# Optimization experiments

Hardware: AMD Instinct MI355X
Metric: run time of the kernel (lower is better)

The kernel has to match this reference:

```python
import jax, jax.numpy as jnp
import numpy as np

H_STEPS = 30 * 24 * 12
HID = 128
BATCH = 16


def setup_inputs() -> dict:
    key = jax.random.key(0)
    ks = jax.random.split(key, 16)
    s = 1.0 / np.sqrt(HID)  # PyTorch LSTM/Linear init scale
    u = lambda k, shape: jax.random.uniform(k, shape, jnp.float32, -s, s)
    return {
        "y0": jax.random.normal(ks[0], (BATCH, 1, 1), jnp.float32),
        "h0": jax.random.normal(ks[1], (2, BATCH, HID), jnp.float32),
        "c0": jax.random.normal(ks[2], (2, BATCH, HID), jnp.float32),
        "W_ih0": u(ks[3], (4 * HID, 1)),
        "W_hh0": u(ks[4], (4 * HID, HID)),
        "b_ih0": u(ks[5], (4 * HID,)),
        "b_hh0": u(ks[6], (4 * HID,)),
        "W_ih1": u(ks[7], (4 * HID, HID)),
        "W_hh1": u(ks[8], (4 * HID, HID)),
        "b_ih1": u(ks[9], (4 * HID,)),
        "b_hh1": u(ks[10], (4 * HID,)),
        "fc_w": u(ks[11], (1, HID)),
        "fc_b": u(ks[12], (1,)),
    }


def _lstm_cell(x, h, c, Wi, Wh, bi, bh):
    # PyTorch gate order: i, f, g, o
    gates = x @ Wi.T + bi + h @ Wh.T + bh  # [B, 4H]
    i, f, g, o = jnp.split(gates, 4, axis=-1)
    c_new = jax.nn.sigmoid(f) * c + jax.nn.sigmoid(i) * jnp.tanh(g)
    h_new = jax.nn.sigmoid(o) * jnp.tanh(c_new)
    return h_new, c_new


def reference(y0, h0, c0, W_ih0, W_hh0, b_ih0, b_hh0,
              W_ih1, W_hh1, b_ih1, b_hh1, fc_w, fc_b):
    def step(carry, _):
        y, h0_, c0_, h1_, c1_ = carry  # y: [B,1]
        h0n, c0n = _lstm_cell(y, h0_, c0_, W_ih0, W_hh0, b_ih0, b_hh0)
        h1n, c1n = _lstm_cell(h0n, h1_, c1_, W_ih1, W_hh1, b_ih1, b_hh1)
        yn = h1n @ fc_w.T + fc_b  # [B,1]
        return (yn, h0n, c0n, h1n, c1n), yn

    carry0 = (y0[:, 0, :], h0[0], c0[0], h0[1], c0[1])
    _, ys = jax.lax.scan(step, carry0, None, length=H_STEPS)  # [H, B, 1]
    return jnp.transpose(ys, (1, 0, 2))  # [B, H, 1]
```

## Files before the change

### kernel.cpp

```cpp
#include <hip/hip_runtime.h>

#define HSTEPS 8640
#define HID 128
#define BATCH 16
#define NTHR 512
#define YRING 192
#define INV127 (1.0f / 127.0f)

typedef __attribute__((ext_vector_type(4))) int i32x4;

static __device__ __forceinline__ float sigm(float x) {
    return __builtin_amdgcn_rcpf(1.0f + __expf(-x));
}
template <int CTRL>
static __device__ __forceinline__ float dppmov(float x) {
    return __int_as_float(
        __builtin_amdgcn_mov_dpp(__float_as_int(x), CTRL, 0xF, 0xF, false));
}
static __device__ __forceinline__ float sum4(float x) {
    x += dppmov<0x121>(x);
    x += dppmov<0x122>(x);
    return x;
}
static __device__ __forceinline__ float red_wave(float x) {
    x += dppmov<0x121>(x);
    x += dppmov<0x122>(x);
    x += dppmov<0x124>(x);
    x += dppmov<0x128>(x);
    float t1 = __int_as_float(__builtin_amdgcn_update_dpp(
        0, __float_as_int(x), 0x142 , 0xA, 0xF, false));
    x += t1;
    float t2 = __int_as_float(__builtin_amdgcn_update_dpp(
        0, __float_as_int(x), 0x143 , 0xC, 0xF, false));
    x += t2;
    return x;
}
static __device__ __forceinline__ float maxwave(float x) {
    x = fmaxf(x, dppmov<0x121>(x));
    x = fmaxf(x, dppmov<0x122>(x));
    x = fmaxf(x, dppmov<0x124>(x));
    x = fmaxf(x, dppmov<0x128>(x));
    float t1 = __int_as_float(__builtin_amdgcn_update_dpp(
        0, __float_as_int(x), 0x142, 0xA, 0xF, false));
    x = fmaxf(x, t1);
    float t2 = __int_as_float(__builtin_amdgcn_update_dpp(
        0, __float_as_int(x), 0x143, 0xC, 0xF, false));
    x = fmaxf(x, t2);
    return x;
}
static __device__ __forceinline__ float swzx16(float x) {
    return __int_as_float(
        __builtin_amdgcn_ds_swizzle(__float_as_int(x), 0x401F));
}

static __device__ __forceinline__ int pack4(const float* v, float inv) {
    int a = (int)__builtin_rintf(v[0] * inv);
    int b = (int)__builtin_rintf(v[1] * inv);
    int c = (int)__builtin_rintf(v[2] * inv);
    int d = (int)__builtin_rintf(v[3] * inv);
    return (a & 0xff) | ((b & 0xff) << 8) | ((c & 0xff) << 16) |
           ((d & 0xff) << 24);
}

static __device__ __forceinline__ void quantrow(const float* rp, int grp,
                                                i32x4& f0, i32x4& f1,
                                                float& sw) {
    float v[32];
#pragma unroll
    for (int j = 0; j < 16; ++j) v[j] = rp[16 * grp + j];
#pragma unroll
    for (int j = 0; j < 16; ++j) v[16 + j] = rp[64 + 16 * grp + j];
    float mx = 1e-20f;
#pragma unroll
    for (int j = 0; j < 32; ++j) mx = fmaxf(mx, __builtin_fabsf(v[j]));
    mx = fmaxf(mx, swzx16(mx));
    mx = fmaxf(mx, __shfl_xor(mx, 32, 64));
    float inv = 127.0f / mx;
    sw = mx * INV127;
    f0 = i32x4{pack4(v, inv), pack4(v + 4, inv), pack4(v + 8, inv),
               pack4(v + 12, inv)};
    f1 = i32x4{pack4(v + 16, inv), pack4(v + 20, inv), pack4(v + 24, inv),
               pack4(v + 28, inv)};
}

#define LOADT(M, T, FA, FB, SS)                                               \
    quantrow((M) + (size_t)(128 * ((T) >> 1) + 16 * (2 * gw + ((T) & 1)) +    \
                            ln15) * HID,                                      \
             grp, FA, FB, SS);

#define CH2(Q, A0, A1, FA, FB)                                                \
    Q = __builtin_amdgcn_mfma_i32_16x16x64_i8((A0), FA, zqi, 0, 0, 0);        \
    Q = __builtin_amdgcn_mfma_i32_16x16x64_i8((A1), FB, (Q), 0, 0, 0);

__global__ __launch_bounds__(NTHR, 2) void lstm2_kernel(
    const float* __restrict__ y0, const float* __restrict__ h0in,
    const float* __restrict__ c0in, const float* __restrict__ Wih0,
    const float* __restrict__ Whh0, const float* __restrict__ bih0,
    const float* __restrict__ bhh0, const float* __restrict__ Wih1,
    const float* __restrict__ Whh1, const float* __restrict__ bih1,
    const float* __restrict__ bhh1, const float* __restrict__ fcw,
    const float* __restrict__ fcb, float* __restrict__ out) {
    const int b = blockIdx.x;
    const int t = threadIdx.x;
    const int wv = t >> 6;
    const int ln = t & 63;
    const int grp = ln >> 4;
    const int ln15 = ln & 15;
    const int gw = wv & 3;
    const bool isX = wv < 4;
    const int jj = ln >> 5;
    const bool isBt = (ln & 16) != 0;
    const int e = 32 * gw + 16 * jj + ln15;
    const float foldc = isBt ? 2.0f : 1.0f;
    const int g1 = isBt ? 2 : 0;

    __shared__ __align__(16) char hsm8[512];
    __shared__ float ypartbuf[4];
    __shared__ float maxb[8];
    __shared__ float ybuf[YRING];

    const i32x4 zqi = {0, 0, 0, 0};

    i32x4 Fq0 = zqi, Fq1 = zqi, Fq2 = zqi, Fq3 = zqi, Fq4 = zqi, Fq5 = zqi,
          Fq6 = zqi, Fq7 = zqi, Fq8 = zqi, Fq9 = zqi, Fq10 = zqi, Fq11 = zqi,
          Fq12 = zqi, Fq13 = zqi, Fq14 = zqi, Fq15 = zqi, Fq16 = zqi,
          Fq17 = zqi, Fq18 = zqi, Fq19 = zqi, Fq20 = zqi, Fq21 = zqi,
          Fq22 = zqi, Fq23 = zqi, Fq24 = zqi, Fq25 = zqi, Fq26 = zqi,
          Fq27 = zqi, Fq28 = zqi, Fq29 = zqi, Fq30 = zqi, Fq31 = zqi;
    i32x4 QA0 = zqi, QA1 = zqi, QA2 = zqi, QA3 = zqi, QA4 = zqi, QA5 = zqi,
          QA6 = zqi, QA7 = zqi;
    i32x4 QB0 = zqi, QB1 = zqi, QB2 = zqi, QB3 = zqi, QB4 = zqi, QB5 = zqi,
          QB6 = zqi, QB7 = zqi;
    float B1c = 0, B2c = 0;
    float E1c = 0, E2c = 0;
    float SAb1 = 0, SAb2 = 0;
    float SAq1 = 0, SAq2 = 0;
    float SBb1 = 0, SBb2 = 0;
    float SBq1 = 0, SBq2 = 0;
    float Cst = 0;

    if (isX) {
        float S0, S1, S2, S3, S4, S5, S6, S7;
        LOADT(Whh0, 0, Fq0, Fq1, S0) LOADT(Whh0, 1, Fq2, Fq3, S1)
        LOADT(Whh0, 2, Fq4, Fq5, S2) LOADT(Whh0, 3, Fq6, Fq7, S3)
        LOADT(Whh0, 4, Fq8, Fq9, S4) LOADT(Whh0, 5, Fq10, Fq11, S5)
        LOADT(Whh0, 6, Fq12, Fq13, S6) LOADT(Whh0, 7, Fq14, Fq15, S7)
        SAb1 = (isBt ? (jj ? S5 : S4) : (jj ? S1 : S0)) * foldc;
        SAb2 = isBt ? (jj ? S7 : S6) : (jj ? S3 : S2);
        B1c = (bih0[g1 * 128 + e] + bhh0[g1 * 128 + e]) * foldc;
        B2c = bih0[(g1 + 1) * 128 + e] + bhh0[(g1 + 1) * 128 + e];
        E1c = Wih0[g1 * 128 + e] * foldc;
        E2c = Wih0[(g1 + 1) * 128 + e];
        Cst = isBt ? 0.f : c0in[b * HID + e];
    } else {
        float S0, S1, S2, S3, S4, S5, S6, S7, S8, S9, S10, S11, S12, S13,
            S14, S15;
        LOADT(Wih1, 0, Fq0, Fq1, S0) LOADT(Wih1, 1, Fq2, Fq3, S1)
        LOADT(Wih1, 2, Fq4, Fq5, S2) LOADT(Wih1, 3, Fq6, Fq7, S3)
        LOADT(Wih1, 4, Fq8, Fq9, S4) LOADT(Wih1, 5, Fq10, Fq11, S5)
        LOADT(Wih1, 6, Fq12, Fq13, S6) LOADT(Wih1, 7, Fq14, Fq15, S7)
        LOADT(Whh1, 0, Fq16, Fq17, S8) LOADT(Whh1, 1, Fq18, Fq19, S9)
        LOADT(Whh1, 2, Fq20, Fq21, S10) LOADT(Whh1, 3, Fq22, Fq23, S11)
        LOADT(Whh1, 4, Fq24, Fq25, S12) LOADT(Whh1, 5, Fq26, Fq27, S13)
        LOADT(Whh1, 6, Fq28, Fq29, S14) LOADT(Whh1, 7, Fq30, Fq31, S15)
        SAq1 = (isBt ? (jj ? S5 : S4) : (jj ? S1 : S0)) * foldc * INV127;
        SAq2 = (isBt ? (jj ? S7 : S6) : (jj ? S3 : S2)) * INV127;
        SBb1 = (isBt ? (jj ? S13 : S12) : (jj ? S9 : S8)) * foldc;
        SBb2 = isBt ? (jj ? S15 : S14) : (jj ? S11 : S10);
        B1c = (bih1[g1 * 128 + e] + bhh1[g1 * 128 + e]) * foldc;
        B2c = bih1[(g1 + 1) * 128 + e] + bhh1[(g1 + 1) * 128 + e];
        E1c = isBt ? 0.f : fcw[e];
        Cst = isBt ? 0.f : c0in[(BATCH + b) * HID + e];
    }

    const float fcb_ = fcb[0];

    float hv_ = 0.f;
    if (t < 128) hv_ = h0in[b * HID + t];
    else if (t < 256) hv_ = h0in[(BATCH + b) * HID + (t - 128)];
    float am = maxwave(__builtin_fabsf(hv_));
    if (ln == 63) maxb[wv] = am;
    if (t < 4) ypartbuf[t] = (t == 0) ? (y0[b] - fcb_) : 0.0f;
    __syncthreads();
    const float bm0 = fmaxf(fmaxf(maxb[0], maxb[1]), 1e-20f);
    const float bm1 = fmaxf(fmaxf(maxb[2], maxb[3]), 1e-20f);
    if (t < 128)
        hsm8[t] = (char)(int)__builtin_rintf(hv_ * (127.0f / bm0));
    else if (t < 256)
        hsm8[256 + (t - 128)] = (char)(int)__builtin_rintf(hv_ * (127.0f / bm1));
    __syncthreads();

    if (isX) {
        SAq1 = SAb1 * (bm0 * INV127);
        SAq2 = SAb2 * (bm0 * INV127);
    } else {
        SBq1 = SBb1 * (bm1 * INV127);
        SBq2 = SBb2 * (bm1 * INV127);
    }

    float* outb = out + (size_t)b * HSTEPS;

    if (isX) {
        i32x4 a0 = *(const i32x4*)&hsm8[16 * grp];
        i32x4 a1 = *(const i32x4*)&hsm8[64 + 16 * grp];
        CH2(QA0, a0, a1, Fq0, Fq1) CH2(QA1, a0, a1, Fq2, Fq3)
        CH2(QA2, a0, a1, Fq4, Fq5) CH2(QA3, a0, a1, Fq6, Fq7)
        CH2(QA4, a0, a1, Fq8, Fq9) CH2(QA5, a0, a1, Fq10, Fq11)
        CH2(QA6, a0, a1, Fq12, Fq13) CH2(QA7, a0, a1, Fq14, Fq15)
    }

    int p = 0;
    int ys = 0;
    int flush_at = YRING;

#pragma unroll 1
    for (int s = 0; s < HSTEPS; ++s) {
        if (isX) {
            float yv = sum4(ypartbuf[ln & 3]) + fcb_;
            if (s > 0) {
                if (t == 0) ybuf[ys] = yv;
                ys = (ys == YRING - 1) ? 0 : ys + 1;
            }
            int a1 = isBt ? (jj ? QA5[0] : QA4[0]) : (jj ? QA1[0] : QA0[0]);
            int a2 = isBt ? (jj ? QA7[0] : QA6[0]) : (jj ? QA3[0] : QA2[0]);
            float G1 = __builtin_fmaf(SAq1, (float)a1,
                                      __builtin_fmaf(E1c, yv, B1c));
            float G2 = __builtin_fmaf(SAq2, (float)a2,
                                      __builtin_fmaf(E2c, yv, B2c));
            float v1 = sigm(G1);
            float v2 = sigm(G2);
            float tg = __builtin_fmaf(2.f, swzx16(v1), -1.f);
            Cst = __builtin_fmaf(v2, Cst, v1 * tg);
            float v3 = sigm(2.f * Cst);
            float th = __builtin_fmaf(2.f, v3, -1.f);
            float h0n = swzx16(v2) * th;
            if (!(ln & 16))
                hsm8[(p ^ 1) * 128 + e] =
                    (char)(int)__builtin_rintf(h0n * 127.0f);
            if (s == 0) {
                SAq1 = SAb1 * INV127;
                SAq2 = SAb2 * INV127;
            }
        } else {
            const char* h1p = hsm8 + 256 + 128 * p + 16 * grp;
            i32x4 b0_ = *(const i32x4*)(h1p);
            i32x4 b1_ = *(const i32x4*)(h1p + 64);
            CH2(QB0, b0_, b1_, Fq16, Fq17) CH2(QB1, b0_, b1_, Fq18, Fq19)
            CH2(QB2, b0_, b1_, Fq20, Fq21) CH2(QB3, b0_, b1_, Fq22, Fq23)
            CH2(QB4, b0_, b1_, Fq24, Fq25) CH2(QB5, b0_, b1_, Fq26, Fq27)
            CH2(QB6, b0_, b1_, Fq28, Fq29) CH2(QB7, b0_, b1_, Fq30, Fq31)
        }
        __syncthreads();

        if (isX) {
            if (s == flush_at) {
                if (t < YRING) outb[flush_at - YRING + t] = ybuf[t];
                flush_at += YRING;
            }
            const char* h0np = hsm8 + (p ^ 1) * 128 + 16 * grp;
            i32x4 d0 = *(const i32x4*)(h0np);
            i32x4 d1 = *(const i32x4*)(h0np + 64);
            CH2(QA0, d0, d1, Fq0, Fq1) CH2(QA1, d0, d1, Fq2, Fq3)
            CH2(QA2, d0, d1, Fq4, Fq5) CH2(QA3, d0, d1, Fq6, Fq7)
            CH2(QA4, d0, d1, Fq8, Fq9) CH2(QA5, d0, d1, Fq10, Fq11)
            CH2(QA6, d0, d1, Fq12, Fq13) CH2(QA7, d0, d1, Fq14, Fq15)
        } else {
            __builtin_amdgcn_s_setprio(1);
            const char* h0np = hsm8 + (p ^ 1) * 128 + 16 * grp;
            i32x4 d0 = *(const i32x4*)(h0np);
            i32x4 d1 = *(const i32x4*)(h0np + 64);
            CH2(QA0, d0, d1, Fq0, Fq1) CH2(QA1, d0, d1, Fq2, Fq3)
            CH2(QA2, d0, d1, Fq4, Fq5) CH2(QA3, d0, d1, Fq6, Fq7)
            CH2(QA4, d0, d1, Fq8, Fq9) CH2(QA5, d0, d1, Fq10, Fq11)
            CH2(QA6, d0, d1, Fq12, Fq13) CH2(QA7, d0, d1, Fq14, Fq15)
            int a1 = isBt ? (jj ? QA5[0] : QA4[0]) : (jj ? QA1[0] : QA0[0]);
            int a2 = isBt ? (jj ? QA7[0] : QA6[0]) : (jj ? QA3[0] : QA2[0]);
            int c1 = isBt ? (jj ? QB5[0] : QB4[0]) : (jj ? QB1[0] : QB0[0]);
            int c2 = isBt ? (jj ? QB7[0] : QB6[0]) : (jj ? QB3[0] : QB2[0]);
            float H1 = __builtin_fmaf(
                SAq1, (float)a1,
                __builtin_fmaf(SBq1, (float)c1, B1c));
            float H2 = __builtin_fmaf(
                SAq2, (float)a2,
                __builtin_fmaf(SBq2, (float)c2, B2c));
            float v1 = sigm(H1);
            float v2 = sigm(H2);
            float tg = __builtin_fmaf(2.f, swzx16(v1), -1.f);
            Cst = __builtin_fmaf(v2, Cst, v1 * tg);
            float v3 = sigm(2.f * Cst);
            float th = __builtin_fmaf(2.f, v3, -1.f);
            float h1n = swzx16(v2) * th;
            __builtin_amdgcn_s_setprio(0);
            if (!(ln & 16))
                hsm8[256 + (p ^ 1) * 128 + e] =
                    (char)(int)__builtin_rintf(h1n * 127.0f);
            float part = red_wave(E1c * h1n);
            if (ln == 63) ypartbuf[gw] = part;
            if (s == 0) {
                SBq1 = SBb1 * INV127;
                SBq2 = SBb2 * INV127;
            }
        }
        __syncthreads();
        p ^= 1;
    }

    if (isX) {
        float yv = sum4(ypartbuf[ln & 3]) + fcb_;
        if (t == 0) ybuf[YRING - 1] = yv;
    }
    __syncthreads();
    if (t < YRING) outb[HSTEPS - YRING + t] = ybuf[t];
}

extern "C" void kernel_launch(void* const* d_in, const int* in_sizes, int n_in,
                              void* d_out, int out_size, void* d_ws,
                              size_t ws_size, hipStream_t stream) {
    const float* y0 = (const float*)d_in[0];
    const float* h0 = (const float*)d_in[1];
    const float* c0 = (const float*)d_in[2];
    const float* Wih0 = (const float*)d_in[3];
    const float* Whh0 = (const float*)d_in[4];
    const float* bih0 = (const float*)d_in[5];
    const float* bhh0 = (const float*)d_in[6];
    const float* Wih1 = (const float*)d_in[7];
    const float* Whh1 = (const float*)d_in[8];
    const float* bih1 = (const float*)d_in[9];
    const float* bhh1 = (const float*)d_in[10];
    const float* fcw = (const float*)d_in[11];
    const float* fcb = (const float*)d_in[12];
    float* out = (float*)d_out;

    lstm2_kernel<<<dim3(BATCH), dim3(NTHR), 0, stream>>>(
        y0, h0, c0, Wih0, Whh0, bih0, bhh0, Wih1, Whh1, bih1, bhh1, fcw, fcb,
        out);
}
```

Baseline: 6.604 ms.

## Quantize layer-1 weights with a shared scale and accumulate both matmuls in MFMA

Layer-1 W_ih1 and W_hh1 rows now share a single int8 scale per row, so the recurrent h1 contribution and the h0 contribution can be summed inside the same int32 MFMA accumulator (the second chain continues from the first instead of being converted separately). This removes a second accumulator set, separate scale factors and extra int-to-float converts and FMAs on the critical layer-1 path. The step-0 term, which uses a different h1 scale, is precomputed before the loop and fed in as a bias. The cost is coarser quantization for whichever matrix has the smaller magnitudes, which may reduce accuracy.

```diff
diff --git a/kernel.cpp b/kernel.cpp
--- a/kernel.cpp
+++ b/kernel.cpp
@@ -83,13 +83,47 @@
                pack4(v + 28, inv)};
 }
 
-#define LOADT(M, T, FA, FB, SS)                                               \
-    quantrow((M) + (size_t)(128 * ((T) >> 1) + 16 * (2 * gw + ((T) & 1)) +    \
-                            ln15) * HID,                                      \
-             grp, FA, FB, SS);
+static __device__ __forceinline__ void quantrow2(const float* rpA,
+                                                 const float* rpB, int grp,
+                                                 i32x4& a0, i32x4& a1,
+                                                 i32x4& b0, i32x4& b1,
+                                                 float& sw) {
+    float vA[32], vB[32];
+#pragma unroll
+    for (int j = 0; j < 16; ++j) {
+        vA[j] = rpA[16 * grp + j];
+        vA[16 + j] = rpA[64 + 16 * grp + j];
+        vB[j] = rpB[16 * grp + j];
+        vB[16 + j] = rpB[64 + 16 * grp + j];
+    }
+    float mx = 1e-20f;
+#pragma unroll
+    for (int j = 0; j < 32; ++j) {
+        mx = fmaxf(mx, __builtin_fabsf(vA[j]));
+        mx = fmaxf(mx, __builtin_fabsf(vB[j]));
+    }
+    mx = fmaxf(mx, swzx16(mx));
+    mx = fmaxf(mx, __shfl_xor(mx, 32, 64));
+    float inv = 127.0f / mx;
+    sw = mx * INV127;
+    a0 = i32x4{pack4(vA, inv), pack4(vA + 4, inv), pack4(vA + 8, inv),
+               pack4(vA + 12, inv)};
+    a1 = i32x4{pack4(vA + 16, inv), pack4(vA + 20, inv), pack4(vA + 24, inv),
+               pack4(vA + 28, inv)};
+    b0 = i32x4{pack4(vB, inv), pack4(vB + 4, inv), pack4(vB + 8, inv),
+               pack4(vB + 12, inv)};
+    b1 = i32x4{pack4(vB + 16, inv), pack4(vB + 20, inv), pack4(vB + 24, inv),
+               pack4(vB + 28, inv)};
+}
+
+#define ROWOFF(T) \
+    ((size_t)(128 * ((T) >> 1) + 16 * (2 * gw + ((T) & 1)) + ln15) * HID)
 
 #define CH2(Q, A0, A1, FA, FB)                                                \
     Q = __builtin_amdgcn_mfma_i32_16x16x64_i8((A0), FA, zqi, 0, 0, 0);        \
+    Q = __builtin_amdgcn_mfma_i32_16x16x64_i8((A1), FB, (Q), 0, 0, 0);
+#define CH2C(Q, A0, A1, FA, FB)                                               \
+    Q = __builtin_amdgcn_mfma_i32_16x16x64_i8((A0), FA, (Q), 0, 0, 0);        \
     Q = __builtin_amdgcn_mfma_i32_16x16x64_i8((A1), FB, (Q), 0, 0, 0);
 
 __global__ __launch_bounds__(NTHR, 2) void lstm2_kernel(
@@ -127,24 +161,25 @@
           Fq17 = zqi, Fq18 = zqi, Fq19 = zqi, Fq20 = zqi, Fq21 = zqi,
           Fq22 = zqi, Fq23 = zqi, Fq24 = zqi, Fq25 = zqi, Fq26 = zqi,
           Fq27 = zqi, Fq28 = zqi, Fq29 = zqi, Fq30 = zqi, Fq31 = zqi;
-    i32x4 QA0 = zqi, QA1 = zqi, QA2 = zqi, QA3 = zqi, QA4 = zqi, QA5 = zqi,
-          QA6 = zqi, QA7 = zqi;
-    i32x4 QB0 = zqi, QB1 = zqi, QB2 = zqi, QB3 = zqi, QB4 = zqi, QB5 = zqi,
-          QB6 = zqi, QB7 = zqi;
+    i32x4 Q0 = zqi, Q1 = zqi, Q2 = zqi, Q3 = zqi, Q4 = zqi, Q5 = zqi,
+          Q6 = zqi, Q7 = zqi;
     float B1c = 0, B2c = 0;
     float E1c = 0, E2c = 0;
     float SAb1 = 0, SAb2 = 0;
     float SAq1 = 0, SAq2 = 0;
-    float SBb1 = 0, SBb2 = 0;
-    float SBq1 = 0, SBq2 = 0;
+    float HB1 = 0, HB2 = 0;
     float Cst = 0;
 
     if (isX) {
         float S0, S1, S2, S3, S4, S5, S6, S7;
-        LOADT(Whh0, 0, Fq0, Fq1, S0) LOADT(Whh0, 1, Fq2, Fq3, S1)
-        LOADT(Whh0, 2, Fq4, Fq5, S2) LOADT(Whh0, 3, Fq6, Fq7, S3)
-        LOADT(Whh0, 4, Fq8, Fq9, S4) LOADT(Whh0, 5, Fq10, Fq11, S5)
-        LOADT(Whh0, 6, Fq12, Fq13, S6) LOADT(Whh0, 7, Fq14, Fq15, S7)
+        quantrow(Whh0 + ROWOFF(0), grp, Fq0, Fq1, S0);
+        quantrow(Whh0 + ROWOFF(1), grp, Fq2, Fq3, S1);
+        quantrow(Whh0 + ROWOFF(2), grp, Fq4, Fq5, S2);
+        quantrow(Whh0 + ROWOFF(3), grp, Fq6, Fq7, S3);
+        quantrow(Whh0 + ROWOFF(4), grp, Fq8, Fq9, S4);
+        quantrow(Whh0 + ROWOFF(5), grp, Fq10, Fq11, S5);
+        quantrow(Whh0 + ROWOFF(6), grp, Fq12, Fq13, S6);
+        quantrow(Whh0 + ROWOFF(7), grp, Fq14, Fq15, S7);
         SAb1 = (isBt ? (jj ? S5 : S4) : (jj ? S1 : S0)) * foldc;
         SAb2 = isBt ? (jj ? S7 : S6) : (jj ? S3 : S2);
         B1c = (bih0[g1 * 128 + e] + bhh0[g1 * 128 + e]) * foldc;
@@ -153,20 +188,27 @@
         E2c = Wih0[(g1 + 1) * 128 + e];
         Cst = isBt ? 0.f : c0in[b * HID + e];
     } else {
-        float S0, S1, S2, S3, S4, S5, S6, S7, S8, S9, S10, S11, S12, S13,
-            S14, S15;
-        LOADT(Wih1, 0, Fq0, Fq1, S0) LOADT(Wih1, 1, Fq2, Fq3, S1)
-        LOADT(Wih1, 2, Fq4, Fq5, S2) LOADT(Wih1, 3, Fq6, Fq7, S3)
-        LOADT(Wih1, 4, Fq8, Fq9, S4) LOADT(Wih1, 5, Fq10, Fq11, S5)
-        LOADT(Wih1, 6, Fq12, Fq13, S6) LOADT(Wih1, 7, Fq14, Fq15, S7)
-        LOADT(Whh1, 0, Fq16, Fq17, S8) LOADT(Whh1, 1, Fq18, Fq19, S9)
-        LOADT(Whh1, 2, Fq20, Fq21, S10) LOADT(Whh1, 3, Fq22, Fq23, S11)
-        LOADT(Whh1, 4, Fq24, Fq25, S12) LOADT(Whh1, 5, Fq26, Fq27, S13)
-        LOADT(Whh1, 6, Fq28, Fq29, S14) LOADT(Whh1, 7, Fq30, Fq31, S15)
-        SAq1 = (isBt ? (jj ? S5 : S4) : (jj ? S1 : S0)) * foldc * INV127;
-        SAq2 = (isBt ? (jj ? S7 : S6) : (jj ? S3 : S2)) * INV127;
-        SBb1 = (isBt ? (jj ? S13 : S12) : (jj ? S9 : S8)) * foldc;
-        SBb2 = isBt ? (jj ? S15 : S14) : (jj ? S11 : S10);
+        float S0, S1, S2, S3, S4, S5, S6, S7;
+        quantrow2(Wih1 + ROWOFF(0), Whh1 + ROWOFF(0), grp, Fq0, Fq1, Fq16,
+                  Fq17, S0);
+        quantrow2(Wih1 + ROWOFF(1), Whh1 + ROWOFF(1), grp, Fq2, Fq3, Fq18,
+                  Fq19, S1);
+        quantrow2(Wih1 + ROWOFF(2), Whh1 + ROWOFF(2), grp, Fq4, Fq5, Fq20,
+                  Fq21, S2);
+        quantrow2(Wih1 + ROWOFF(3), Whh1 + ROWOFF(3), grp, Fq6, Fq7, Fq22,
+                  Fq23, S3);
+        quantrow2(Wih1 + ROWOFF(4), Whh1 + ROWOFF(4), grp, Fq8, Fq9, Fq24,
+                  Fq25, S4);
+        quantrow2(Wih1 + ROWOFF(5), Whh1 + ROWOFF(5), grp, Fq10, Fq11, Fq26,
+                  Fq27, S5);
+        quantrow2(Wih1 + ROWOFF(6), Whh1 + ROWOFF(6), grp, Fq12, Fq13, Fq28,
+                  Fq29, S6);
+        quantrow2(Wih1 + ROWOFF(7), Whh1 + ROWOFF(7), grp, Fq14, Fq15, Fq30,
+                  Fq31, S7);
+        SAb1 = (isBt ? (jj ? S5 : S4) : (jj ? S1 : S0)) * foldc;
+        SAb2 = isBt ? (jj ? S7 : S6) : (jj ? S3 : S2);
+        SAq1 = SAb1 * INV127;
+        SAq2 = SAb2 * INV127;
         B1c = (bih1[g1 * 128 + e] + bhh1[g1 * 128 + e]) * foldc;
         B2c = bih1[(g1 + 1) * 128 + e] + bhh1[(g1 + 1) * 128 + e];
         E1c = isBt ? 0.f : fcw[e];
@@ -190,23 +232,31 @@
         hsm8[256 + (t - 128)] = (char)(int)__builtin_rintf(hv_ * (127.0f / bm1));
     __syncthreads();
 
+    float* outb = out + (size_t)b * HSTEPS;
+
     if (isX) {
         SAq1 = SAb1 * (bm0 * INV127);
         SAq2 = SAb2 * (bm0 * INV127);
-    } else {
-        SBq1 = SBb1 * (bm1 * INV127);
-        SBq2 = SBb2 * (bm1 * INV127);
-    }
-
-    float* outb = out + (size_t)b * HSTEPS;
-
-    if (isX) {
         i32x4 a0 = *(const i32x4*)&hsm8[16 * grp];
         i32x4 a1 = *(const i32x4*)&hsm8[64 + 16 * grp];
-        CH2(QA0, a0, a1, Fq0, Fq1) CH2(QA1, a0, a1, Fq2, Fq3)
-        CH2(QA2, a0, a1, Fq4, Fq5) CH2(QA3, a0, a1, Fq6, Fq7)
-        CH2(QA4, a0, a1, Fq8, Fq9) CH2(QA5, a0, a1, Fq10, Fq11)
-        CH2(QA6, a0, a1, Fq12, Fq13) CH2(QA7, a0, a1, Fq14, Fq15)
+        CH2(Q0, a0, a1, Fq0, Fq1) CH2(Q1, a0, a1, Fq2, Fq3)
+        CH2(Q2, a0, a1, Fq4, Fq5) CH2(Q3, a0, a1, Fq6, Fq7)
+        CH2(Q4, a0, a1, Fq8, Fq9) CH2(Q5, a0, a1, Fq10, Fq11)
+        CH2(Q6, a0, a1, Fq12, Fq13) CH2(Q7, a0, a1, Fq14, Fq15)
+    } else {
+        i32x4 b0_ = *(const i32x4*)&hsm8[256 + 16 * grp];
+        i32x4 b1_ = *(const i32x4*)&hsm8[256 + 64 + 16 * grp];
+        i32x4 T0, T1, T2, T3, T4, T5, T6, T7;
+        CH2(T0, b0_, b1_, Fq16, Fq17) CH2(T1, b0_, b1_, Fq18, Fq19)
+        CH2(T2, b0_, b1_, Fq20, Fq21) CH2(T3, b0_, b1_, Fq22, Fq23)
+        CH2(T4, b0_, b1_, Fq24, Fq25) CH2(T5, b0_, b1_, Fq26, Fq27)
+        CH2(T6, b0_, b1_, Fq28, Fq29) CH2(T7, b0_, b1_, Fq30, Fq31)
+        int a1s = isBt ? (jj ? T5[0] : T4[0]) : (jj ? T1[0] : T0[0]);
+        int a2s = isBt ? (jj ? T7[0] : T6[0]) : (jj ? T3[0] : T2[0]);
+        HB1 = SAb1 * (bm1 * INV127) * (float)a1s;
+        HB2 = SAb2 * (bm1 * INV127) * (float)a2s;
+        Q0 = zqi; Q1 = zqi; Q2 = zqi; Q3 = zqi;
+        Q4 = zqi; Q5 = zqi; Q6 = zqi; Q7 = zqi;
     }
 
     int p = 0;
@@ -221,8 +271,8 @@
                 if (t == 0) ybuf[ys] = yv;
                 ys = (ys == YRING - 1) ? 0 : ys + 1;
             }
-            int a1 = isBt ? (jj ? QA5[0] : QA4[0]) : (jj ? QA1[0] : QA0[0]);
-            int a2 = isBt ? (jj ? QA7[0] : QA6[0]) : (jj ? QA3[0] : QA2[0]);
+            int a1 = isBt ? (jj ? Q5[0] : Q4[0]) : (jj ? Q1[0] : Q0[0]);
+            int a2 = isBt ? (jj ? Q7[0] : Q6[0]) : (jj ? Q3[0] : Q2[0]);
             float G1 = __builtin_fmaf(SAq1, (float)a1,
                                       __builtin_fmaf(E1c, yv, B1c));
             float G2 = __builtin_fmaf(SAq2, (float)a2,
@@ -241,14 +291,14 @@
                 SAq1 = SAb1 * INV127;
                 SAq2 = SAb2 * INV127;
             }
-        } else {
+        } else if (s > 0) {
             const char* h1p = hsm8 + 256 + 128 * p + 16 * grp;
             i32x4 b0_ = *(const i32x4*)(h1p);
             i32x4 b1_ = *(const i32x4*)(h1p + 64);
-            CH2(QB0, b0_, b1_, Fq16, Fq17) CH2(QB1, b0_, b1_, Fq18, Fq19)
-            CH2(QB2, b0_, b1_, Fq20, Fq21) CH2(QB3, b0_, b1_, Fq22, Fq23)
-            CH2(QB4, b0_, b1_, Fq24, Fq25) CH2(QB5, b0_, b1_, Fq26, Fq27)
-            CH2(QB6, b0_, b1_, Fq28, Fq29) CH2(QB7, b0_, b1_, Fq30, Fq31)
+            CH2(Q0, b0_, b1_, Fq16, Fq17) CH2(Q1, b0_, b1_, Fq18, Fq19)
+            CH2(Q2, b0_, b1_, Fq20, Fq21) CH2(Q3, b0_, b1_, Fq22, Fq23)
+            CH2(Q4, b0_, b1_, Fq24, Fq25) CH2(Q5, b0_, b1_, Fq26, Fq27)
+            CH2(Q6, b0_, b1_, Fq28, Fq29) CH2(Q7, b0_, b1_, Fq30, Fq31)
         }
         __syncthreads();
 
@@ -260,29 +310,23 @@
             const char* h0np = hsm8 + (p ^ 1) * 128 + 16 * grp;
             i32x4 d0 = *(const i32x4*)(h0np);
             i32x4 d1 = *(const i32x4*)(h0np + 64);
-            CH2(QA0, d0, d1, Fq0, Fq1) CH2(QA1, d0, d1, Fq2, Fq3)
-            CH2(QA2, d0, d1, Fq4, Fq5) CH2(QA3, d0, d1, Fq6, Fq7)
-            CH2(QA4, d0, d1, Fq8, Fq9) CH2(QA5, d0, d1, Fq10, Fq11)
-            CH2(QA6, d0, d1, Fq12, Fq13) CH2(QA7, d0, d1, Fq14, Fq15)
+            CH2(Q0, d0, d1, Fq0, Fq1) CH2(Q1, d0, d1, Fq2, Fq3)
+            CH2(Q2, d0, d1, Fq4, Fq5) CH2(Q3, d0, d1, Fq6, Fq7)
+            CH2(Q4, d0, d1, Fq8, Fq9) CH2(Q5, d0, d1, Fq10, Fq11)
+            CH2(Q6, d0, d1, Fq12, Fq13) CH2(Q7, d0, d1, Fq14, Fq15)
         } else {
             __builtin_amdgcn_s_setprio(1);
             const char* h0np = hsm8 + (p ^ 1) * 128 + 16 * grp;
             i32x4 d0 = *(const i32x4*)(h0np);
             i32x4 d1 = *(const i32x4*)(h0np + 64);
-            CH2(QA0, d0, d1, Fq0, Fq1) CH2(QA1, d0, d1, Fq2, Fq3)
-            CH2(QA2, d0, d1, Fq4, Fq5) CH2(QA3, d0, d1, Fq6, Fq7)
-            CH2(QA4, d0, d1, Fq8, Fq9) CH2(QA5, d0, d1, Fq10, Fq11)
-            CH2(QA6, d0, d1, Fq12, Fq13) CH2(QA7, d0, d1, Fq14, Fq15)
-            int a1 = isBt ? (jj ? QA5[0] : QA4[0]) : (jj ? QA1[0] : QA0[0]);
-            int a2 = isBt ? (jj ? QA7[0] : QA6[0]) : (jj ? QA3[0] : QA2[0]);
-            int c1 = isBt ? (jj ? QB5[0] : QB4[0]) : (jj ? QB1[0] : QB0[0]);
-            int c2 = isBt ? (jj ? QB7[0] : QB6[0]) : (jj ? QB3[0] : QB2[0]);
-            float H1 = __builtin_fmaf(
-                SAq1, (float)a1,
-                __builtin_fmaf(SBq1, (float)c1, B1c));
-            float H2 = __builtin_fmaf(
-                SAq2, (float)a2,
-                __builtin_fmaf(SBq2, (float)c2, B2c));
+            CH2C(Q0, d0, d1, Fq0, Fq1) CH2C(Q1, d0, d1, Fq2, Fq3)
+            CH2C(Q2, d0, d1, Fq4, Fq5) CH2C(Q3, d0, d1, Fq6, Fq7)
+            CH2C(Q4, d0, d1, Fq8, Fq9) CH2C(Q5, d0, d1, Fq10, Fq11)
+            CH2C(Q6, d0, d1, Fq12, Fq13) CH2C(Q7, d0, d1, Fq14, Fq15)
+            int a1 = isBt ? (jj ? Q5[0] : Q4[0]) : (jj ? Q1[0] : Q0[0]);
+            int a2 = isBt ? (jj ? Q7[0] : Q6[0]) : (jj ? Q3[0] : Q2[0]);
+            float H1 = __builtin_fmaf(SAq1, (float)a1, B1c + HB1);
+            float H2 = __builtin_fmaf(SAq2, (float)a2, B2c + HB2);
             float v1 = sigm(H1);
             float v2 = sigm(H2);
             float tg = __builtin_fmaf(2.f, swzx16(v1), -1.f);
@@ -297,8 +341,8 @@
             float part = red_wave(E1c * h1n);
             if (ln == 63) ypartbuf[gw] = part;
             if (s == 0) {
-                SBq1 = SBb1 * INV127;
-                SBq2 = SBb2 * INV127;
+                HB1 = 0.f;
+                HB2 = 0.f;
             }
         }
         __syncthreads();
```

Measured after the change: 6.083 ms. -7.9%, faster.
